# Optimization experiments

Hardware: AMD Instinct MI355X
Metric: run time of the kernel (lower is better)

The kernel has to match this reference:

```python
import jax, jax.numpy as jnp
import numpy as np
from jax import lax


def _lstm_layer(x, h0, c0, W_ih, W_hh, b_ih, b_hh):
    # x: [B,T,I]; precompute input projection for all timesteps: [B,T,4H]
    xg = jnp.einsum('bti,gi->btg', x, W_ih) + b_ih

    def step(carry, xg_t):
        h, c = carry
        gates = xg_t + h @ W_hh.T + b_hh  # [B,4H]
        i, f, g, o = jnp.split(gates, 4, axis=-1)  # PyTorch LSTMCell gate order
        i = jax.nn.sigmoid(i)
        f = jax.nn.sigmoid(f)
        g = jnp.tanh(g)
        o = jax.nn.sigmoid(o)
        c = f * c + i * g
        h = o * jnp.tanh(c)
        return (h, c), h

    (h, c), ys = lax.scan(step, (h0, c0), jnp.swapaxes(xg, 0, 1))  # scan over T
    return jnp.swapaxes(ys, 0, 1), h, c  # [B,T,H], [B,H], [B,H]


def setup_inputs() -> dict:
    key = jax.random.key(0)
    ks = jax.random.split(key, 10)
    B, T, I, H = 128, 256, 256, 1024
    s = 0.02
    return {
        'x': jax.random.normal(ks[0], (B, T, I), jnp.float32),
        'hx0': jnp.zeros((2, B, H), jnp.float32),
        'cx0': jnp.zeros((2, B, H), jnp.float32),
        'W_ih0': jax.random.normal(ks[1], (4 * H, I), jnp.float32) * s,
        'W_hh0': jax.random.normal(ks[2], (4 * H, H), jnp.float32) * s,
        'b_ih0': jax.random.normal(ks[3], (4 * H,), jnp.float32) * s,
        'b_hh0': jax.random.normal(ks[4], (4 * H,), jnp.float32) * s,
        'W_ih1': jax.random.normal(ks[5], (4 * H, H), jnp.float32) * s,
        'W_hh1': jax.random.normal(ks[6], (4 * H, H), jnp.float32) * s,
        'b_ih1': jax.random.normal(ks[7], (4 * H,), jnp.float32) * s,
        'b_hh1': jax.random.normal(ks[8], (4 * H,), jnp.float32) * s,
    }


def reference(x, hx0, cx0, W_ih0, W_hh0, b_ih0, b_hh0, W_ih1, W_hh1, b_ih1, b_hh1):
    # Eval mode / variational_inference=False with dropout=0.0: masks are exact ones.
    x, h, c = _lstm_layer(x, hx0[0], cx0[0], W_ih0, W_hh0, b_ih0, b_hh0)
    x, h, c = _lstm_layer(x, hx0[1], cx0[1], W_ih1, W_hh1, b_ih1, b_hh1)
    return x, h, c
```

## Files before the change

kernel.cpp:

```cpp
#include <hip/hip_runtime.h>

typedef __attribute__((ext_vector_type(8))) short short8;
typedef __attribute__((ext_vector_type(4))) float f32x4;

#define DEV static __device__ __forceinline__

DEV unsigned short f2b(float f) {
    union { float f; unsigned u; } v; v.f = f;
    unsigned r = (v.u + 0x7FFFu + ((v.u >> 16) & 1u)) >> 16;
    return (unsigned short)r;
}
DEV float b2f(unsigned short s) {
    union { unsigned u; float f; } v; v.u = ((unsigned)s) << 16;
    return v.f;
}
DEV float sigm(float x) { return 1.0f / (1.0f + __expf(-x)); }


__global__ void k_f2b(const float* __restrict__ src, unsigned short* __restrict__ dst, int n4) {
    int i = blockIdx.x * blockDim.x + threadIdx.x;
    if (i < n4) {
        float4 v = ((const float4*)src)[i];
        ushort4 o;
        o.x = f2b(v.x); o.y = f2b(v.y); o.z = f2b(v.z); o.w = f2b(v.w);
        ((ushort4*)dst)[i] = o;
    }
}

__global__ void k_perm(const float* __restrict__ src, unsigned short* __restrict__ dst, int Kq) {
    int i = blockIdx.x * blockDim.x + threadIdx.x;
    int total = 4096 * Kq;
    if (i >= total) return;
    int rp = i / Kq, kq = i - rp * Kq;
    int j = rp >> 2, g = rp & 3;
    float4 v = ((const float4*)src)[(size_t)(g * 1024 + j) * Kq + kq];
    ushort4 o;
    o.x = f2b(v.x); o.y = f2b(v.y); o.z = f2b(v.z); o.w = f2b(v.w);
    ((ushort4*)dst)[(size_t)rp * Kq + kq] = o;
}

__global__ void k_bias(const float* __restrict__ bi0, const float* __restrict__ bh0,
                       const float* __restrict__ bi1, const float* __restrict__ bh1,
                       float* __restrict__ d0, float* __restrict__ d1) {
    int i = blockIdx.x * blockDim.x + threadIdx.x;
    if (i < 4096) {
        int j = i >> 2, g = i & 3, s = g * 1024 + j;
        d0[i] = bi0[s] + bh0[s];
        d1[i] = bi1[s] + bh1[s];
    }
}

__global__ void k_init(const float* __restrict__ hx, const float* __restrict__ cx,
                       unsigned* __restrict__ hB0, unsigned* __restrict__ hB1,
                       float* __restrict__ c0, float* __restrict__ c1) {
    int i = blockIdx.x * blockDim.x + threadIdx.x;
    if (i < 128 * 512) {
        int b = i >> 9, j = i & 511;
        const float* p0 = hx + (size_t)b * 1024 + j * 2;
        const float* p1 = hx + 131072 + (size_t)b * 1024 + j * 2;
        hB0[i] = (unsigned)f2b(p0[0]) | ((unsigned)f2b(p0[1]) << 16);
        hB1[i] = (unsigned)f2b(p1[0]) | ((unsigned)f2b(p1[1]) << 16);
        c0[i * 2] = cx[i * 2];
        c0[i * 2 + 1] = cx[i * 2 + 1];
        c1[i * 2] = cx[131072 + i * 2];
        c1[i * 2 + 1] = cx[131072 + i * 2 + 1];
    }
}

__global__ __launch_bounds__(256) void k_gemm(
    const unsigned short* __restrict__ A, const unsigned short* __restrict__ W,
    unsigned short* __restrict__ out, int K, int t0, int TC) {
    __shared__ unsigned short ldsA[128 * 40];
    __shared__ unsigned short ldsB[128 * 40];
    const int tid = threadIdx.x;
    const int w = tid >> 6, l = tid & 63;
    const int wm = w >> 1, wn = w & 1;
    const int bm = blockIdx.x, bn = blockIdx.y;
    const int lr = l & 15, lk = (l >> 4) * 8;

    const int row0 = tid >> 2, inb = (tid & 3) << 4;
    const int row1 = row0 + 64;
    const int v0 = bm * 128 + row0, v1 = bm * 128 + row1;
    const size_t ar0 = (size_t)((v0 / TC) * 256 + t0 + (v0 % TC));
    const size_t ar1 = (size_t)((v1 / TC) * 256 + t0 + (v1 % TC));
    const size_t br0 = (size_t)(bn * 128 + row0);
    const size_t br1 = (size_t)(bn * 128 + row1);

    f32x4 acc[4][4];
#pragma unroll
    for (int a = 0; a < 4; a++)
#pragma unroll
        for (int b = 0; b < 4; b++) acc[a][b] = (f32x4){0.f, 0.f, 0.f, 0.f};

    for (int ks = 0; ks < K; ks += 32) {
        uint4 a0 = *(const uint4*)((const char*)A + (ar0 * K + ks) * 2 + inb);
        uint4 a1 = *(const uint4*)((const char*)A + (ar1 * K + ks) * 2 + inb);
        uint4 b0 = *(const uint4*)((const char*)W + (br0 * K + ks) * 2 + inb);
        uint4 b1 = *(const uint4*)((const char*)W + (br1 * K + ks) * 2 + inb);
        *(uint4*)((char*)ldsA + row0 * 80 + inb) = a0;
        *(uint4*)((char*)ldsA + row1 * 80 + inb) = a1;
        *(uint4*)((char*)ldsB + row0 * 80 + inb) = b0;
        *(uint4*)((char*)ldsB + row1 * 80 + inb) = b1;
        __syncthreads();
        short8 af[4], bf[4];
#pragma unroll
        for (int mt = 0; mt < 4; mt++)
            af[mt] = *(const short8*)((const char*)ldsA + (wm * 64 + mt * 16 + lr) * 80 + lk * 2);
#pragma unroll
        for (int nt = 0; nt < 4; nt++)
            bf[nt] = *(const short8*)((const char*)ldsB + (wn * 64 + nt * 16 + lr) * 80 + lk * 2);
#pragma unroll
        for (int mt = 0; mt < 4; mt++)
#pragma unroll
            for (int nt = 0; nt < 4; nt++)
                acc[mt][nt] = __builtin_amdgcn_mfma_f32_16x16x32_bf16(af[mt], bf[nt], acc[mt][nt], 0, 0, 0);
        __syncthreads();
    }

#pragma unroll
    for (int mt = 0; mt < 4; mt++)
#pragma unroll
        for (int nt = 0; nt < 4; nt++)
#pragma unroll
            for (int v4 = 0; v4 < 4; v4++) {
                int vr = bm * 128 + wm * 64 + mt * 16 + (l >> 4) * 4 + v4;
                int col = bn * 128 + wn * 64 + nt * 16 + lr;
                out[(size_t)vr * 4096 + col] = f2b(acc[mt][nt][v4]);
            }
}

template<int LAYER>
__global__ __launch_bounds__(512, 2) void k_lstm(
    const unsigned short* __restrict__ Wh,
    const unsigned short* __restrict__ xg,
    const float* __restrict__ bias,
    float* __restrict__ cbuf,
    unsigned* __restrict__ hA,
    unsigned* __restrict__ hB,
    unsigned short* __restrict__ y0,
    float* __restrict__ out,
    unsigned* __restrict__ flags,
    int t0, int TC)
{
    extern __shared__ char smem[];
    unsigned short* ldsW = (unsigned short*)smem;
    float* P0 = (float*)(smem + 64 * 2064);
    float* P1 = P0 + 16 * 132;
    float* P2 = P1 + 16 * 132;

    const int tid = threadIdx.x;
    const int g  = (int)blockIdx.x >> 5;
    const int nb = (int)blockIdx.x & 31;
    const int w  = tid >> 6;
    const int l  = tid & 63;
    const int lr = l & 15, lq = l >> 4;

    {
        const char* src = (const char*)(Wh + (size_t)nb * 128 * 1024);
#pragma unroll
        for (int it = 0; it < 16; it++) {
            int idx = it * 512 + tid;
            int row = idx >> 7, inr = (idx & 127) << 4;
            *(uint4*)(smem + row * 2064 + inr) = *(const uint4*)(src + (size_t)row * 2048 + inr);
        }
    }
    short8 wreg[16];
    {
        const unsigned short* src = Wh + (size_t)(nb * 128 + 64) * 1024 + w * 128;
#pragma unroll
        for (int ct = 0; ct < 4; ct++)
#pragma unroll
            for (int kk = 0; kk < 4; kk++)
                wreg[ct * 4 + kk] =
                    *(const short8*)(src + (size_t)(ct * 16 + lr) * 1024 + kk * 32 + lq * 8);
    }

    const int er = tid >> 4, ep = tid & 15;
    const int eb = g * 16 + (er & 15);
    const int ec0 = nb * 128 + ep * 8;
    const int eu0 = nb * 32 + ep * 2;
    float2 c2 = make_float2(0.f, 0.f);
    float4 bsA = make_float4(0.f, 0.f, 0.f, 0.f);
    float4 bsB = make_float4(0.f, 0.f, 0.f, 0.f);
    if (tid < 256) {
        c2 = *(const float2*)(cbuf + (size_t)eb * 1024 + eu0);
        bsA = *(const float4*)(bias + ec0);
        bsB = *(const float4*)(bias + ec0 + 4);
    }

    const size_t abase = (size_t)(g * 16 + lr) * 256 + (size_t)w * 32 + lq * 2;
    const char* wp = (const char*)ldsW + (size_t)lr * 2064 + w * 256 + lq * 16;

    const unsigned* fpw = flags + (size_t)(g * 32 + w * 4 + (l & 3)) * 16;
    unsigned* fmine = flags + (size_t)(g * 32 + nb) * 16;

    __syncthreads();

    for (int dt = 0; dt < TC; dt++) {
        const int t = t0 + dt;
        uint4 xv = make_uint4(0, 0, 0, 0);
        if (tid < 256)
            xv = *(const uint4*)(xg + (size_t)eb * ((size_t)TC * 4096) + (size_t)dt * 4096 + ec0);

        if (t > 0) {
            const unsigned tgt = (unsigned)t;
            while (!__all(__hip_atomic_load(fpw, __ATOMIC_RELAXED,
                                            __HIP_MEMORY_SCOPE_AGENT) >= tgt)) {}
        }

        const unsigned long long* ap =
            (const unsigned long long*)((t & 1) ? hA : hB) + abase;
        f32x4 acc[8];
#pragma unroll
        for (int i = 0; i < 8; i++) acc[i] = (f32x4){0.f, 0.f, 0.f, 0.f};
#pragma unroll
        for (int kk = 0; kk < 4; kk++) {
            union { unsigned long long u[2]; short8 s; } av;
            av.u[0] = __hip_atomic_load(ap + kk * 8,     __ATOMIC_RELAXED, __HIP_MEMORY_SCOPE_AGENT);
            av.u[1] = __hip_atomic_load(ap + kk * 8 + 1, __ATOMIC_RELAXED, __HIP_MEMORY_SCOPE_AGENT);
#pragma unroll
            for (int ct = 0; ct < 4; ct++) {
                short8 b = *(const short8*)(wp + (size_t)ct * 16 * 2064 + kk * 64);
                acc[ct] = __builtin_amdgcn_mfma_f32_16x16x32_bf16(av.s, b, acc[ct], 0, 0, 0);
            }
#pragma unroll
            for (int ct = 0; ct < 4; ct++)
                acc[4 + ct] = __builtin_amdgcn_mfma_f32_16x16x32_bf16(av.s, wreg[ct * 4 + kk], acc[4 + ct], 0, 0, 0);
        }

        if (w >= 5) {
            float* P = (w == 5) ? P0 : (w == 6) ? P1 : P2;
#pragma unroll
            for (int i = 0; i < 8; i++)
#pragma unroll
                for (int v = 0; v < 4; v++)
                    P[(lq * 4 + v) * 132 + i * 16 + lr] = acc[i][v];
        }
        __syncthreads();
        if (w >= 2 && w <= 4) {
            float* P = (w == 2) ? P0 : (w == 3) ? P1 : P2;
#pragma unroll
            for (int i = 0; i < 8; i++)
#pragma unroll
                for (int v = 0; v < 4; v++)
                    P[(lq * 4 + v) * 132 + i * 16 + lr] += acc[i][v];
        }
        __syncthreads();
        if (w < 2) {
            float* P = (w == 0) ? P0 : P1;
#pragma unroll
            for (int i = 0; i < 8; i++)
#pragma unroll
                for (int v = 0; v < 4; v++)
                    P[(lq * 4 + v) * 132 + i * 16 + lr] += acc[i][v];
        }
        __syncthreads();

        float h0v = 0.f, h1v = 0.f;
        if (tid < 256) {
            const float* pa = P0 + er * 132 + ep * 8;
            const float* pb = P1 + er * 132 + ep * 8;
            const float* pc = P2 + er * 132 + ep * 8;
            const unsigned short* xs = (const unsigned short*)&xv;
            float p0 = pa[0] + pb[0] + pc[0] + b2f(xs[0]) + bsA.x;
            float p1 = pa[1] + pb[1] + pc[1] + b2f(xs[1]) + bsA.y;
            float p2 = pa[2] + pb[2] + pc[2] + b2f(xs[2]) + bsA.z;
            float p3 = pa[3] + pb[3] + pc[3] + b2f(xs[3]) + bsA.w;
            float q0 = pa[4] + pb[4] + pc[4] + b2f(xs[4]) + bsB.x;
            float q1 = pa[5] + pb[5] + pc[5] + b2f(xs[5]) + bsB.y;
            float q2 = pa[6] + pb[6] + pc[6] + b2f(xs[6]) + bsB.z;
            float q3 = pa[7] + pb[7] + pc[7] + b2f(xs[7]) + bsB.w;
            float i0 = sigm(p0), f0 = sigm(p1), gv0 = tanhf(p2), o0 = sigm(p3);
            float i1 = sigm(q0), f1 = sigm(q1), gv1 = tanhf(q2), o1 = sigm(q3);
            c2.x = f0 * c2.x + i0 * gv0;
            c2.y = f1 * c2.y + i1 * gv1;
            h0v = o0 * tanhf(c2.x);
            h1v = o1 * tanhf(c2.y);
            unsigned hp = (unsigned)f2b(h0v) | ((unsigned)f2b(h1v) << 16);
            unsigned* hout = (t & 1) ? hB : hA;
            __hip_atomic_store(hout + (size_t)eb * 512 + eu0 / 2, hp,
                               __ATOMIC_RELAXED, __HIP_MEMORY_SCOPE_AGENT);
        }
        __syncthreads();
        if (tid == 0)
            __hip_atomic_store(fmine, (unsigned)(t + 1),
                               __ATOMIC_RELAXED, __HIP_MEMORY_SCOPE_AGENT);

        if (tid < 256) {
            if (LAYER == 0) {
                unsigned hp = (unsigned)f2b(h0v) | ((unsigned)f2b(h1v) << 16);
                ((unsigned*)y0)[((size_t)eb * 256 + t) * 512 + eu0 / 2] = hp;
            } else {
                *(float2*)(out + ((size_t)eb * 256 + t) * 1024 + eu0) = make_float2(h0v, h1v);
                if (t == 255) {
                    *(float2*)(out + (size_t)128 * 256 * 1024 + (size_t)eb * 1024 + eu0) =
                        make_float2(h0v, h1v);
                    *(float2*)(out + (size_t)128 * 256 * 1024 + (size_t)128 * 1024 + (size_t)eb * 1024 + eu0) =
                        make_float2(c2.x, c2.y);
                }
            }
        }
    }
    if (tid < 256)
        *(float2*)(cbuf + (size_t)eb * 1024 + eu0) = c2;
}


extern "C" void kernel_launch(void* const* d_in, const int* in_sizes, int n_in,
                              void* d_out, int out_size, void* d_ws, size_t ws_size,
                              hipStream_t stream) {
    const float* x    = (const float*)d_in[0];
    const float* hx0  = (const float*)d_in[1];
    const float* cx0  = (const float*)d_in[2];
    const float* Wih0 = (const float*)d_in[3];
    const float* Whh0 = (const float*)d_in[4];
    const float* bih0 = (const float*)d_in[5];
    const float* bhh0 = (const float*)d_in[6];
    const float* Wih1 = (const float*)d_in[7];
    const float* Whh1 = (const float*)d_in[8];
    const float* bih1 = (const float*)d_in[9];
    const float* bhh1 = (const float*)d_in[10];
    float* out = (float*)d_out;

    const int B = 128, T = 256, I = 256, H = 1024, G4 = 4096;
    const unsigned SMEM_BYTES = 64 * 2064 + 3 * 16 * 132 * 4;
    const int FLAGS_U32 = 8 * 32 * 16;

    hipFuncSetAttribute((const void*)&k_lstm<0>, hipFuncAttributeMaxDynamicSharedMemorySize, SMEM_BYTES);
    hipFuncSetAttribute((const void*)&k_lstm<1>, hipFuncAttributeMaxDynamicSharedMemorySize, SMEM_BYTES);

    char* p = (char*)d_ws;
    auto alloc = [&](size_t bytes) { char* r = p; p += (bytes + 255) & ~(size_t)255; return r; };
    unsigned short* xbf   = (unsigned short*)alloc((size_t)B * T * I * 2);
    unsigned short* Wih0p = (unsigned short*)alloc((size_t)G4 * I * 2);
    unsigned short* Whh0p = (unsigned short*)alloc((size_t)G4 * H * 2);
    unsigned short* Wih1p = (unsigned short*)alloc((size_t)G4 * H * 2);
    unsigned short* Whh1p = (unsigned short*)alloc((size_t)G4 * H * 2);
    float* bias0 = (float*)alloc(G4 * 4);
    float* bias1 = (float*)alloc(G4 * 4);
    unsigned short* y0 = (unsigned short*)alloc((size_t)B * T * H * 2);
    unsigned* hA0 = (unsigned*)alloc((size_t)B * 512 * 4);
    unsigned* hB0 = (unsigned*)alloc((size_t)B * 512 * 4);
    unsigned* hA1 = (unsigned*)alloc((size_t)B * 512 * 4);
    unsigned* hB1 = (unsigned*)alloc((size_t)B * 512 * 4);
    float* c0 = (float*)alloc((size_t)B * H * 4);
    float* c1 = (float*)alloc((size_t)B * H * 4);
    unsigned* flags0 = (unsigned*)alloc((size_t)2 * FLAGS_U32 * 4);
    unsigned* flags1 = flags0 + FLAGS_U32;
    size_t fixed = (size_t)(p - (char*)d_ws);
    int TC = 256;
    while (TC > 1 && fixed + (size_t)B * TC * G4 * 2 + 256 > ws_size) TC >>= 1;
    unsigned short* xg = (unsigned short*)alloc((size_t)B * TC * G4 * 2);

    hipMemsetAsync(flags0, 0, (size_t)2 * FLAGS_U32 * 4, stream);
    k_f2b<<<(B * T * I / 4 + 255) / 256, 256, 0, stream>>>(x, xbf, B * T * I / 4);
    k_perm<<<(G4 * (I / 4) + 255) / 256, 256, 0, stream>>>(Wih0, Wih0p, I / 4);
    k_perm<<<(G4 * (H / 4) + 255) / 256, 256, 0, stream>>>(Whh0, Whh0p, H / 4);
    k_perm<<<(G4 * (H / 4) + 255) / 256, 256, 0, stream>>>(Wih1, Wih1p, H / 4);
    k_perm<<<(G4 * (H / 4) + 255) / 256, 256, 0, stream>>>(Whh1, Whh1p, H / 4);
    k_bias<<<16, 256, 0, stream>>>(bih0, bhh0, bih1, bhh1, bias0, bias1);
    k_init<<<256, 256, 0, stream>>>(hx0, cx0, hB0, hB1, c0, c1);

    for (int t0 = 0; t0 < T; t0 += TC) {
        k_gemm<<<dim3(TC, 32), 256, 0, stream>>>(xbf, Wih0p, xg, I, t0, TC);
        int t0v = t0, TCv = TC;
        const unsigned short* Whp = Whh0p;
        const unsigned short* xgp = xg;
        const float* bp = bias0;
        float* cp = c0;
        unsigned* ha = hA0; unsigned* hb = hB0;
        unsigned short* y0p = y0;
        float* op = nullptr;
        unsigned* fl = flags0;
        void* args[] = {&Whp, &xgp, &bp, &cp, &ha, &hb, &y0p, &op, &fl, &t0v, &TCv};
        hipLaunchCooperativeKernel((const void*)&k_lstm<0>, dim3(256), dim3(512), args, SMEM_BYTES, stream);
    }
    for (int t0 = 0; t0 < T; t0 += TC) {
        k_gemm<<<dim3(TC, 32), 256, 0, stream>>>(y0, Wih1p, xg, H, t0, TC);
        int t0v = t0, TCv = TC;
        const unsigned short* Whp = Whh1p;
        const unsigned short* xgp = xg;
        const float* bp = bias1;
        float* cp = c1;
        unsigned* ha = hA1; unsigned* hb = hB1;
        unsigned short* y0p = nullptr;
        float* op = out;
        unsigned* fl = flags1;
        void* args[] = {&Whp, &xgp, &bp, &cp, &ha, &hb, &y0p, &op, &fl, &t0v, &TCv};
        hipLaunchCooperativeKernel((const void*)&k_lstm<1>, dim3(256), dim3(512), args, SMEM_BYTES, stream);
    }
}
```

Measured before the change: 3.046 ms.

## Use direct global-to-LDS loads with XOR swizzle in GEMM; remap LSTM block grid

The input-projection GEMM now stages A and B tiles with global_load_lds (direct global-to-LDS DMA) instead of loading into registers and storing to LDS. LDS rows become 64 bytes with an XOR swizzle on the 16-byte chunk index to avoid bank conflicts in place of padding. The recurrent kernel swaps the block-index mapping so that batch groups vary fastest, and each wave now polls all 32 producer flags of its group instead of a per-wave subset. The added risks are a constraint on LDS destination layout from the direct-load path and more spin-polling traffic on the flags.

```diff
diff --git a/kernel.cpp b/kernel.cpp
--- a/kernel.cpp
+++ b/kernel.cpp
@@ -70,21 +70,26 @@
 __global__ __launch_bounds__(256) void k_gemm(
     const unsigned short* __restrict__ A, const unsigned short* __restrict__ W,
     unsigned short* __restrict__ out, int K, int t0, int TC) {
-    __shared__ unsigned short ldsA[128 * 40];
-    __shared__ unsigned short ldsB[128 * 40];
+    __shared__ char ldsA[128 * 64];
+    __shared__ char ldsB[128 * 64];
     const int tid = threadIdx.x;
     const int w = tid >> 6, l = tid & 63;
     const int wm = w >> 1, wn = w & 1;
     const int bm = blockIdx.x, bn = blockIdx.y;
-    const int lr = l & 15, lk = (l >> 4) * 8;
-
-    const int row0 = tid >> 2, inb = (tid & 3) << 4;
-    const int row1 = row0 + 64;
+    const int lr = l & 15, lkq = l >> 4;
+
+    const int row0 = w * 16 + (l >> 2);
+    const int row1 = (w + 4) * 16 + (l >> 2);
+    const int qq = l & 3;
+    const int inb0 = ((qq ^ (row0 & 3)) << 4);
+    const int inb1 = ((qq ^ (row1 & 3)) << 4);
     const int v0 = bm * 128 + row0, v1 = bm * 128 + row1;
     const size_t ar0 = (size_t)((v0 / TC) * 256 + t0 + (v0 % TC));
     const size_t ar1 = (size_t)((v1 / TC) * 256 + t0 + (v1 % TC));
-    const size_t br0 = (size_t)(bn * 128 + row0);
-    const size_t br1 = (size_t)(bn * 128 + row1);
+    const char* baseA0 = (const char*)A + ar0 * K * 2 + inb0;
+    const char* baseA1 = (const char*)A + ar1 * K * 2 + inb1;
+    const char* baseB0 = (const char*)W + (size_t)(bn * 128 + row0) * K * 2 + inb0;
+    const char* baseB1 = (const char*)W + (size_t)(bn * 128 + row1) * K * 2 + inb1;
 
     f32x4 acc[4][4];
 #pragma unroll
@@ -93,22 +98,30 @@
         for (int b = 0; b < 4; b++) acc[a][b] = (f32x4){0.f, 0.f, 0.f, 0.f};
 
     for (int ks = 0; ks < K; ks += 32) {
-        uint4 a0 = *(const uint4*)((const char*)A + (ar0 * K + ks) * 2 + inb);
-        uint4 a1 = *(const uint4*)((const char*)A + (ar1 * K + ks) * 2 + inb);
-        uint4 b0 = *(const uint4*)((const char*)W + (br0 * K + ks) * 2 + inb);
-        uint4 b1 = *(const uint4*)((const char*)W + (br1 * K + ks) * 2 + inb);
-        *(uint4*)((char*)ldsA + row0 * 80 + inb) = a0;
-        *(uint4*)((char*)ldsA + row1 * 80 + inb) = a1;
-        *(uint4*)((char*)ldsB + row0 * 80 + inb) = b0;
-        *(uint4*)((char*)ldsB + row1 * 80 + inb) = b1;
+        __builtin_amdgcn_global_load_lds(
+            (const __attribute__((address_space(1))) unsigned*)(baseA0 + (size_t)ks * 2),
+            (__attribute__((address_space(3))) unsigned*)(ldsA + w * 1024), 16, 0, 0);
+        __builtin_amdgcn_global_load_lds(
+            (const __attribute__((address_space(1))) unsigned*)(baseA1 + (size_t)ks * 2),
+            (__attribute__((address_space(3))) unsigned*)(ldsA + (w + 4) * 1024), 16, 0, 0);
+        __builtin_amdgcn_global_load_lds(
+            (const __attribute__((address_space(1))) unsigned*)(baseB0 + (size_t)ks * 2),
+            (__attribute__((address_space(3))) unsigned*)(ldsB + w * 1024), 16, 0, 0);
+        __builtin_amdgcn_global_load_lds(
+            (const __attribute__((address_space(1))) unsigned*)(baseB1 + (size_t)ks * 2),
+            (__attribute__((address_space(3))) unsigned*)(ldsB + (w + 4) * 1024), 16, 0, 0);
         __syncthreads();
         short8 af[4], bf[4];
 #pragma unroll
-        for (int mt = 0; mt < 4; mt++)
-            af[mt] = *(const short8*)((const char*)ldsA + (wm * 64 + mt * 16 + lr) * 80 + lk * 2);
-#pragma unroll
-        for (int nt = 0; nt < 4; nt++)
-            bf[nt] = *(const short8*)((const char*)ldsB + (wn * 64 + nt * 16 + lr) * 80 + lk * 2);
+        for (int mt = 0; mt < 4; mt++) {
+            int row = wm * 64 + mt * 16 + lr;
+            af[mt] = *(const short8*)(ldsA + row * 64 + ((lkq ^ (row & 3)) << 4));
+        }
+#pragma unroll
+        for (int nt = 0; nt < 4; nt++) {
+            int row = wn * 64 + nt * 16 + lr;
+            bf[nt] = *(const short8*)(ldsB + row * 64 + ((lkq ^ (row & 3)) << 4));
+        }
 #pragma unroll
         for (int mt = 0; mt < 4; mt++)
 #pragma unroll
@@ -143,15 +156,15 @@
     int t0, int TC)
 {
     extern __shared__ char smem[];
-    unsigned short* ldsW = (unsigned short*)smem;
+    char* ldsW = smem;
     float* P0 = (float*)(smem + 64 * 2064);
     float* P1 = P0 + 16 * 132;
     float* P2 = P1 + 16 * 132;
 
     const int tid = threadIdx.x;
-    const int g  = (int)blockIdx.x >> 5;
-    const int nb = (int)blockIdx.x & 31;
-    const int w  = tid >> 6;
+    const int g  = (int)blockIdx.x & 7;
+    const int nb = (int)blockIdx.x >> 3;
+    const int wv = tid >> 6;
     const int l  = tid & 63;
     const int lr = l & 15, lq = l >> 4;
 
@@ -161,12 +174,12 @@
         for (int it = 0; it < 16; it++) {
             int idx = it * 512 + tid;
             int row = idx >> 7, inr = (idx & 127) << 4;
-            *(uint4*)(smem + row * 2064 + inr) = *(const uint4*)(src + (size_t)row * 2048 + inr);
+            *(uint4*)(ldsW + row * 2064 + inr) = *(const uint4*)(src + (size_t)row * 2048 + inr);
         }
     }
     short8 wreg[16];
     {
-        const unsigned short* src = Wh + (size_t)(nb * 128 + 64) * 1024 + w * 128;
+        const unsigned short* src = Wh + (size_t)(nb * 128 + 64) * 1024 + wv * 128;
 #pragma unroll
         for (int ct = 0; ct < 4; ct++)
 #pragma unroll
@@ -188,10 +201,10 @@
         bsB = *(const float4*)(bias + ec0 + 4);
     }
 
-    const size_t abase = (size_t)(g * 16 + lr) * 256 + (size_t)w * 32 + lq * 2;
-    const char* wp = (const char*)ldsW + (size_t)lr * 2064 + w * 256 + lq * 16;
-
-    const unsigned* fpw = flags + (size_t)(g * 32 + w * 4 + (l & 3)) * 16;
+    const size_t abase = (size_t)(g * 16 + lr) * 256 + (size_t)wv * 32 + lq * 2;
+    const char* wp = ldsW + (size_t)lr * 2064 + wv * 256 + lq * 16;
+
+    const unsigned* fp = flags + (size_t)(g * 32 + (l & 31)) * 16;
     unsigned* fmine = flags + (size_t)(g * 32 + nb) * 16;
 
     __syncthreads();
@@ -204,7 +217,7 @@
 
         if (t > 0) {
             const unsigned tgt = (unsigned)t;
-            while (!__all(__hip_atomic_load(fpw, __ATOMIC_RELAXED,
+            while (!__all(__hip_atomic_load(fp, __ATOMIC_RELAXED,
                                             __HIP_MEMORY_SCOPE_AGENT) >= tgt)) {}
         }
 
@@ -228,8 +241,8 @@
                 acc[4 + ct] = __builtin_amdgcn_mfma_f32_16x16x32_bf16(av.s, wreg[ct * 4 + kk], acc[4 + ct], 0, 0, 0);
         }
 
-        if (w >= 5) {
-            float* P = (w == 5) ? P0 : (w == 6) ? P1 : P2;
+        if (wv >= 5) {
+            float* P = (wv == 5) ? P0 : (wv == 6) ? P1 : P2;
 #pragma unroll
             for (int i = 0; i < 8; i++)
 #pragma unroll
@@ -237,8 +250,8 @@
                     P[(lq * 4 + v) * 132 + i * 16 + lr] = acc[i][v];
         }
         __syncthreads();
-        if (w >= 2 && w <= 4) {
-            float* P = (w == 2) ? P0 : (w == 3) ? P1 : P2;
+        if (wv >= 2 && wv <= 4) {
+            float* P = (wv == 2) ? P0 : (wv == 3) ? P1 : P2;
 #pragma unroll
             for (int i = 0; i < 8; i++)
 #pragma unroll
@@ -246,8 +259,8 @@
                     P[(lq * 4 + v) * 132 + i * 16 + lr] += acc[i][v];
         }
         __syncthreads();
-        if (w < 2) {
-            float* P = (w == 0) ? P0 : P1;
+        if (wv < 2) {
+            float* P = (wv == 0) ? P0 : P1;
 #pragma unroll
             for (int i = 0; i < 8; i++)
 #pragma unroll
```

After: 3.330 ms. +9.3%, slower.
